# Performance work log

Measured on AMD Instinct MI355X. Metric: run time of the kernel, lower is better.

## Reference

```python
import jax, jax.numpy as jnp
import numpy as np

WS = 7           # window size
N = WS * WS      # tokens per window = 49
C = 128          # embed dim
H = 4            # heads
HD = C // H      # head dim = 32
NW = 64          # num windows (mask leading dim)
B = 4096         # total windows = outer_batch * NW


def _relative_indexes():
    ch = np.arange(WS)
    cw = np.arange(WS)
    coords = np.stack(np.meshgrid(ch, cw, indexing='ij')).reshape(2, -1)  # [2, N]
    rel = coords[:, :, None] - coords[:, None, :]                          # [2, N, N]
    rel = rel.transpose(1, 2, 0)
    rel[:, :, 0] += WS - 1
    rel[:, :, 1] += WS - 1
    rel[:, :, 0] *= 2 * WS - 1
    return jnp.asarray(rel.sum(-1), dtype=jnp.int32)                       # [N, N]


def setup_inputs() -> dict:
    key = jax.random.key(0)
    ks = jax.random.split(key, 10)
    s = 0.02
    return {
        'query': jax.random.normal(ks[0], (B, N, C), jnp.float32),
        'source': jax.random.normal(ks[1], (B, N, C), jnp.float32),
        'mask': jnp.zeros((NW, N, N), jnp.float32),
        'q_w': jax.random.normal(ks[2], (C, C), jnp.float32) * s,
        'q_b': jnp.zeros((C,), jnp.float32),
        'kv_w': jax.random.normal(ks[3], (C, 2 * C), jnp.float32) * s,
        'kv_b': jnp.zeros((2 * C,), jnp.float32),
        'proj_w': jax.random.normal(ks[4], (C, C), jnp.float32) * s,
        'proj_b': jnp.zeros((C,), jnp.float32),
        'bias_table': jax.random.normal(ks[5], ((2 * WS - 1) ** 2, H), jnp.float32) * s,
        'rel_idx': _relative_indexes(),
    }


def reference(query, source, mask, q_w, q_b, kv_w, kv_b, proj_w, proj_b, bias_table, rel_idx):
    scale = HD ** -0.5
    q = query @ q_w + q_b                       # [B, N, C]
    kv = source @ kv_w + kv_b                   # [B, N, 2C]
    k, v = kv[..., :C], kv[..., C:]
    # [B, N, H, HD] -> [B, H, N, HD]
    q = q.reshape(B, N, H, HD).transpose(0, 2, 1, 3) * scale
    k = k.reshape(B, N, H, HD).transpose(0, 2, 1, 3)
    v = v.reshape(B, N, H, HD).transpose(0, 2, 1, 3)
    attn = jnp.einsum('bhnd,bhmd->bhnm', q, k)  # [B, H, N, N]
    # gathered relative positional bias: [1, H, N, N]
    bias = bias_table[rel_idx.reshape(-1)].reshape(N, N, H).transpose(2, 0, 1)[None]
    attn = attn + bias
    # mask: [NW, N, N] broadcast over outer batch and heads
    attn = attn.reshape(-1, NW, H, N, N) + mask[None, :, None]
    attn = attn.reshape(B, H, N, N)
    attn = jax.nn.softmax(attn, axis=-1)
    x = jnp.einsum('bhnm,bhmd->bnhd', attn, v).reshape(B, N, C)
    return x @ proj_w + proj_b
```

## Files before the change

### kernel.cpp

```cpp
#include <hip/hip_runtime.h>
#include <hip/hip_bf16.h>

#define NN 49
#define CC 128
#define HH 4
#define NWIN 64
#define BB 4096
#define QSCALE 0.17677669529663687f

typedef __attribute__((ext_vector_type(8))) short bf16x8;
typedef __attribute__((ext_vector_type(4))) float f32x4;
typedef unsigned short u16;
typedef unsigned int u32;

union U8 { u32 u[4]; bf16x8 v; };

__device__ __forceinline__ u16 f2b(float f) {
    __hip_bfloat16 h = __float2bfloat16(f);
    return __builtin_bit_cast(u16, h);
}
__device__ __forceinline__ float b2f(u16 u) { return __uint_as_float(((u32)u) << 16); }
__device__ __forceinline__ u32 cvtpk(float lo, float hi) {
    u32 r;
    asm("v_cvt_pk_bf16_f32 %0, %1, %2" : "=v"(r) : "v"(lo), "v"(hi));
    return r;
}
__device__ __forceinline__ uint2 pack4(float a, float b, float c, float d) {
    uint2 r;
    r.x = cvtpk(a, b);
    r.y = cvtpk(c, d);
    return r;
}
__device__ __forceinline__ f32x4 mfma16(bf16x8 a, bf16x8 b, f32x4 c) {
    return __builtin_amdgcn_mfma_f32_16x16x32_bf16(a, b, c, 0, 0, 0);
}
__device__ __forceinline__ char* adr256(u16* base, int row, int byte) {
    return (char*)base + row * 256 + (byte ^ ((row & 7) << 4));
}
__device__ __forceinline__ char* adr128(u16* base, int row, int byte) {
    return (char*)base + row * 128 + (byte ^ ((row & 7) << 4));
}

__global__ void prep_cbt(const float* __restrict__ bias_table, const int* __restrict__ rel_idx,
                         const float* __restrict__ mask, u16* __restrict__ cbt) {
    int idx = blockIdx.x * blockDim.x + threadIdx.x;
    int m = idx & 63, i = (idx >> 6) & 63, h = (idx >> 12) & 3, wv = idx >> 14;
    if (wv >= NWIN) return;
    float v = -1e9f;
    if (m < NN && i < NN)
        v = bias_table[rel_idx[i * NN + m] * HH + h] + mask[(wv * NN + i) * NN + m];
    cbt[idx] = f2b(v);
}

__global__ void prep_w(const float* __restrict__ qw, const float* __restrict__ qb,
                       const float* __restrict__ kvw, const float* __restrict__ pjw,
                       u16* __restrict__ qwp, u16* __restrict__ kvwp,
                       u16* __restrict__ pjwp, float* __restrict__ qbs) {
    int idx = blockIdx.x * blockDim.x + threadIdx.x;
    if (idx < 16384) {
        int i = idx & 7, lane = (idx >> 3) & 63, kt = (idx >> 9) & 3, nt = idx >> 11;
        int k = 32 * kt + 8 * (lane >> 4) + i, n = 16 * nt + (lane & 15);
        qwp[idx] = f2b(qw[k * CC + n] * QSCALE);
    } else if (idx < 49152) {
        int j = idx - 16384;
        int i = j & 7, lane = (j >> 3) & 63, kt = (j >> 9) & 3, nt = j >> 11;
        int k = 32 * kt + 8 * (lane >> 4) + i, n = 16 * nt + (lane & 15);
        kvwp[j] = f2b(kvw[k * 2 * CC + n]);
    } else if (idx < 65536) {
        int j = idx - 49152;
        int i = j & 7, lane = (j >> 3) & 63, kt = (j >> 9) & 3, nt = j >> 11;
        int k = 32 * kt + 8 * (lane >> 4) + i, n = 16 * nt + (lane & 15);
        pjwp[j] = f2b(pjw[k * CC + n]);
    } else if (idx < 65664) {
        int j = idx - 65536;
        qbs[j] = qb[j] * QSCALE;
    }
}

__global__ __launch_bounds__(512, 2)
void wmha_main(const float* __restrict__ query, const float* __restrict__ source,
               const u16* __restrict__ qwp, const u16* __restrict__ kvwp,
               const u16* __restrict__ pjwp, const float* __restrict__ qbs,
               const float* __restrict__ kv_b, const float* __restrict__ proj_b,
               const u16* __restrict__ cbt, float* __restrict__ out) {
    __shared__ u16 lds[40960];
    u16* SQ = lds;
    u16* SS = lds + 8192;
    u16* Qb = lds + 16384;
    u16* Kb = lds + 24576;
    u16* VT = lds + 32768;
    const int t = threadIdx.x;
    const int b = blockIdx.x;
    const int w = t >> 6, lane = t & 63;
    const int lq = lane & 15, qd = lane >> 4;
    const int mw = w >> 2;
    const int nw = w & 3;
    const int h = w >> 1;
    const int half = w & 1;

    {
        const int row = t >> 3, qu = t & 7;
        const size_t gbase = (size_t)b * NN * CC + row * CC + qu * 8;
        #pragma unroll
        for (int j = 0; j < 2; ++j) {
            U8 vq, vs;
            if (row < NN) {
                const float4* q4 = (const float4*)(query + gbase) + 16 * j;
                const float4* s4 = (const float4*)(source + gbase) + 16 * j;
                float4 a0 = q4[0], a1 = q4[1], c0 = s4[0], c1 = s4[1];
                vq.u[0] = cvtpk(a0.x, a0.y); vq.u[1] = cvtpk(a0.z, a0.w);
                vq.u[2] = cvtpk(a1.x, a1.y); vq.u[3] = cvtpk(a1.z, a1.w);
                vs.u[0] = cvtpk(c0.x, c0.y); vs.u[1] = cvtpk(c0.z, c0.w);
                vs.u[2] = cvtpk(c1.x, c1.y); vs.u[3] = cvtpk(c1.z, c1.w);
            } else {
                vq.u[0] = vq.u[1] = vq.u[2] = vq.u[3] = 0;
                vs.u[0] = vs.u[1] = vs.u[2] = vs.u[3] = 0;
            }
            *(bf16x8*)adr256(SQ, row, qu * 16 + 128 * j) = vq.v;
            *(bf16x8*)adr256(SS, row, qu * 16 + 128 * j) = vs.v;
        }
    }
    bf16x8 bwq[2][4];
    #pragma unroll
    for (int n2 = 0; n2 < 2; ++n2)
        #pragma unroll
        for (int kt = 0; kt < 4; ++kt)
            bwq[n2][kt] = *(const bf16x8*)(qwp + (((nw + 4 * n2) * 4 + kt) * 64 + lane) * 8);
    __syncthreads();

    {
        f32x4 acc[2][2] = {};
        #pragma unroll
        for (int m2 = 0; m2 < 2; ++m2) {
            bf16x8 a[4];
            #pragma unroll
            for (int kt = 0; kt < 4; ++kt)
                a[kt] = *(const bf16x8*)adr256(SQ, (2 * mw + m2) * 16 + lq, kt * 64 + qd * 16);
            __builtin_amdgcn_s_setprio(1);
            #pragma unroll
            for (int n2 = 0; n2 < 2; ++n2)
                #pragma unroll
                for (int kt = 0; kt < 4; ++kt)
                    acc[m2][n2] = mfma16(bwq[n2][kt], a[kt], acc[m2][n2]);
            __builtin_amdgcn_s_setprio(0);
        }
        #pragma unroll
        for (int n2 = 0; n2 < 2; ++n2) {
            const int cb0 = 16 * (nw + 4 * n2) + 4 * qd;
            const float4 bia = *(const float4*)(qbs + cb0);
            #pragma unroll
            for (int m2 = 0; m2 < 2; ++m2) {
                const int tok = (2 * mw + m2) * 16 + lq;
                uint2 pk = pack4(acc[m2][n2][0] + bia.x, acc[m2][n2][1] + bia.y,
                                 acc[m2][n2][2] + bia.z, acc[m2][n2][3] + bia.w);
                *(uint2*)adr256(Qb, tok, 2 * cb0) = pk;
            }
        }
    }
    {
        bf16x8 as[2][4];
        #pragma unroll
        for (int m2 = 0; m2 < 2; ++m2)
            #pragma unroll
            for (int kt = 0; kt < 4; ++kt)
                as[m2][kt] = *(const bf16x8*)adr256(SS, (2 * mw + m2) * 16 + lq, kt * 64 + qd * 16);
        {
            bf16x8 bwk[2][4];
            #pragma unroll
            for (int n2 = 0; n2 < 2; ++n2)
                #pragma unroll
                for (int kt = 0; kt < 4; ++kt)
                    bwk[n2][kt] = *(const bf16x8*)(kvwp + (((nw + 4 * n2) * 4 + kt) * 64 + lane) * 8);
            f32x4 acc[2][2] = {};
            __builtin_amdgcn_s_setprio(1);
            #pragma unroll
            for (int m2 = 0; m2 < 2; ++m2)
                #pragma unroll
                for (int n2 = 0; n2 < 2; ++n2)
                    #pragma unroll
                    for (int kt = 0; kt < 4; ++kt)
                        acc[m2][n2] = mfma16(bwk[n2][kt], as[m2][kt], acc[m2][n2]);
            __builtin_amdgcn_s_setprio(0);
            #pragma unroll
            for (int n2 = 0; n2 < 2; ++n2) {
                const int cb0 = 16 * (nw + 4 * n2) + 4 * qd;
                const float4 bia = *(const float4*)(kv_b + cb0);
                #pragma unroll
                for (int m2 = 0; m2 < 2; ++m2) {
                    const int tok = (2 * mw + m2) * 16 + lq;
                    uint2 pk = pack4(acc[m2][n2][0] + bia.x, acc[m2][n2][1] + bia.y,
                                     acc[m2][n2][2] + bia.z, acc[m2][n2][3] + bia.w);
                    *(uint2*)adr256(Kb, tok, 2 * cb0) = pk;
                }
            }
        }
        {
            bf16x8 bwv[2][4];
            #pragma unroll
            for (int n2 = 0; n2 < 2; ++n2)
                #pragma unroll
                for (int kt = 0; kt < 4; ++kt)
                    bwv[n2][kt] = *(const bf16x8*)(kvwp + (((8 + nw + 4 * n2) * 4 + kt) * 64 + lane) * 8);
            f32x4 acc[2][2] = {};
            __builtin_amdgcn_s_setprio(1);
            #pragma unroll
            for (int m2 = 0; m2 < 2; ++m2)
                #pragma unroll
                for (int n2 = 0; n2 < 2; ++n2)
                    #pragma unroll
                    for (int kt = 0; kt < 4; ++kt)
                        acc[m2][n2] = mfma16(as[m2][kt], bwv[n2][kt], acc[m2][n2]);
            __builtin_amdgcn_s_setprio(0);
            #pragma unroll
            for (int n2 = 0; n2 < 2; ++n2) {
                const int dim = 16 * (nw + 4 * n2) + lq;
                const float bias = kv_b[CC + dim];
                #pragma unroll
                for (int m2 = 0; m2 < 2; ++m2) {
                    uint2 pk = pack4(acc[m2][n2][0] + bias, acc[m2][n2][1] + bias,
                                     acc[m2][n2][2] + bias, acc[m2][n2][3] + bias);
                    *(uint2*)adr128(VT, dim, 2 * ((2 * mw + m2) * 16 + qd * 4)) = pk;
                }
            }
        }
    }
    __syncthreads();

    f32x4 s[2][4];
    bf16x8 vf[2][2];
    {
        bf16x8 kf[4], qf[2];
        #pragma unroll
        for (int a = 0; a < 4; ++a)
            kf[a] = *(const bf16x8*)adr256(Kb, a * 16 + lq, h * 64 + qd * 16);
        #pragma unroll
        for (int i = 0; i < 2; ++i)
            qf[i] = *(const bf16x8*)adr256(Qb, (2 * half + i) * 16 + lq, h * 64 + qd * 16);
        __builtin_amdgcn_s_setprio(1);
        #pragma unroll
        for (int i = 0; i < 2; ++i) {
            f32x4 z = {0.f, 0.f, 0.f, 0.f};
            #pragma unroll
            for (int a = 0; a < 4; ++a)
                s[i][a] = mfma16(kf[a], qf[i], z);
        }
        __builtin_amdgcn_s_setprio(0);
        #pragma unroll
        for (int dt = 0; dt < 2; ++dt)
            #pragma unroll
            for (int kt = 0; kt < 2; ++kt)
                vf[dt][kt] = *(const bf16x8*)adr128(VT, h * 32 + dt * 16 + lq, kt * 64 + qd * 16);
    }
    uint2 cbr[2][4];
    {
        const u16* cbb = cbt + ((size_t)((b & (NWIN - 1)) * HH + h) << 12);
        #pragma unroll
        for (int i = 0; i < 2; ++i)
            #pragma unroll
            for (int a = 0; a < 4; ++a)
                cbr[i][a] = *(const uint2*)(cbb + ((2 * half + i) * 16 + lq) * 64 + a * 16 + qd * 4);
    }
    __syncthreads();

    {
        u16* pb0 = Qb + w * 1024;
        u16* pb1 = Kb + w * 1024;
        float smv[2];
        #pragma unroll
        for (int i = 0; i < 2; ++i) {
            #pragma unroll
            for (int a = 0; a < 3; ++a) {
                s[i][a][0] += b2f((u16)(cbr[i][a].x & 0xffffu));
                s[i][a][1] += b2f((u16)(cbr[i][a].x >> 16));
                s[i][a][2] += b2f((u16)(cbr[i][a].y & 0xffffu));
                s[i][a][3] += b2f((u16)(cbr[i][a].y >> 16));
            }
            s[i][3][0] += b2f((u16)(cbr[i][3].x & 0xffffu));
            uint2 pk[4];
            float sm = 0.f;
            #pragma unroll
            for (int a = 0; a < 3; ++a) {
                float p0 = __expf(s[i][a][0]), p1 = __expf(s[i][a][1]);
                float p2 = __expf(s[i][a][2]), p3 = __expf(s[i][a][3]);
                pk[a].x = cvtpk(p0, p1);
                pk[a].y = cvtpk(p2, p3);
                sm += (p0 + p1) + (p2 + p3);
            }
            float p30 = __expf(s[i][3][0]);
            pk[3].x = cvtpk(p30, 0.f);
            pk[3].y = 0u;
            sm += p30;
            smv[i] = sm;
            u16* pb = i ? pb1 : pb0;
            #pragma unroll
            for (int a = 0; a < 4; ++a)
                *(uint2*)adr128(pb, lq, 32 * a + 8 * qd) = pk[a];
        }
        asm volatile("s_waitcnt lgkmcnt(0)" ::: "memory");
        __builtin_amdgcn_sched_barrier(0);
        float t0 = smv[0] + __shfl_xor(smv[0], 16);
        float t1 = smv[1] + __shfl_xor(smv[1], 16);
        float inv[2];
        inv[0] = 1.f / (t0 + __shfl_xor(t0, 32));
        inv[1] = 1.f / (t1 + __shfl_xor(t1, 32));
        f32x4 o[2][2] = {};
        __builtin_amdgcn_s_setprio(1);
        #pragma unroll
        for (int kt = 0; kt < 2; ++kt) {
            bf16x8 pf0 = *(const bf16x8*)adr128(pb0, lq, 64 * kt + 16 * qd);
            bf16x8 pf1 = *(const bf16x8*)adr128(pb1, lq, 64 * kt + 16 * qd);
            #pragma unroll
            for (int dt = 0; dt < 2; ++dt) {
                o[0][dt] = mfma16(vf[dt][kt], pf0, o[0][dt]);
                o[1][dt] = mfma16(vf[dt][kt], pf1, o[1][dt]);
            }
        }
        __builtin_amdgcn_s_setprio(0);
        #pragma unroll
        for (int i = 0; i < 2; ++i)
            #pragma unroll
            for (int dt = 0; dt < 2; ++dt) {
                uint2 px = pack4(o[i][dt][0] * inv[i], o[i][dt][1] * inv[i],
                                 o[i][dt][2] * inv[i], o[i][dt][3] * inv[i]);
                *(uint2*)adr256(SQ, (2 * half + i) * 16 + lq, 64 * h + 32 * dt + 8 * qd) = px;
            }
    }

    {
        bf16x8 bw[2][4];
        #pragma unroll
        for (int n2 = 0; n2 < 2; ++n2)
            #pragma unroll
            for (int kt = 0; kt < 4; ++kt)
                bw[n2][kt] = *(const bf16x8*)(pjwp + (((nw + 4 * n2) * 4 + kt) * 64 + lane) * 8);
        __syncthreads();
        f32x4 acc[2][2] = {};
        #pragma unroll
        for (int m2 = 0; m2 < 2; ++m2) {
            bf16x8 a[4];
            #pragma unroll
            for (int kt = 0; kt < 4; ++kt)
                a[kt] = *(const bf16x8*)adr256(SQ, (2 * mw + m2) * 16 + lq, kt * 64 + qd * 16);
            __builtin_amdgcn_s_setprio(1);
            #pragma unroll
            for (int n2 = 0; n2 < 2; ++n2)
                #pragma unroll
                for (int kt = 0; kt < 4; ++kt)
                    acc[m2][n2] = mfma16(bw[n2][kt], a[kt], acc[m2][n2]);
            __builtin_amdgcn_s_setprio(0);
        }
        float* outb = out + (size_t)b * NN * CC;
        #pragma unroll
        for (int n2 = 0; n2 < 2; ++n2) {
            const int cb0 = 16 * (nw + 4 * n2) + 4 * qd;
            const float4 bia = *(const float4*)(proj_b + cb0);
            #pragma unroll
            for (int m2 = 0; m2 < 2; ++m2) {
                const int tok = (2 * mw + m2) * 16 + lq;
                if (tok < NN) {
                    float4 vst;
                    vst.x = acc[m2][n2][0] + bia.x;
                    vst.y = acc[m2][n2][1] + bia.y;
                    vst.z = acc[m2][n2][2] + bia.z;
                    vst.w = acc[m2][n2][3] + bia.w;
                    *(float4*)(outb + tok * CC + cb0) = vst;
                }
            }
        }
    }
}

extern "C" void kernel_launch(void* const* d_in, const int* in_sizes, int n_in,
                              void* d_out, int out_size, void* d_ws, size_t ws_size,
                              hipStream_t stream) {
    const float* query      = (const float*)d_in[0];
    const float* source     = (const float*)d_in[1];
    const float* mask       = (const float*)d_in[2];
    const float* q_w        = (const float*)d_in[3];
    const float* q_b        = (const float*)d_in[4];
    const float* kv_w       = (const float*)d_in[5];
    const float* kv_b       = (const float*)d_in[6];
    const float* proj_w     = (const float*)d_in[7];
    const float* proj_b     = (const float*)d_in[8];
    const float* bias_table = (const float*)d_in[9];
    const int*   rel_idx    = (const int*)d_in[10];
    float* out = (float*)d_out;

    u16* cbt   = (u16*)d_ws;
    u16* qwp   = cbt + 1048576;
    u16* kvwp  = qwp + 16384;
    u16* pjwp  = kvwp + 32768;
    float* qbs = (float*)(pjwp + 16384);

    prep_cbt<<<4096, 256, 0, stream>>>(bias_table, rel_idx, mask, cbt);
    prep_w<<<257, 256, 0, stream>>>(q_w, q_b, kv_w, proj_w, qwp, kvwp, pjwp, qbs);
    wmha_main<<<BB, 512, 0, stream>>>(query, source, qwp, kvwp, pjwp, qbs,
                                      kv_b, proj_b, cbt, out);
}
```

Before: 122.3 us.

## Make blocks persistent over 8 windows with register prefetch of next window

Each block now loops over 8 windows instead of one, and the grid shrinks to 512 blocks. During each window, the next window's query and source rows are loaded into registers so the global load latency overlaps with the softmax and PV stage. The attention output is now staged in VT so SQ/SS can be refilled early. This adds register pressure from the prefetch buffers and extra syncs. With only 512 blocks, the machine may be underfilled and load per CU may be uneven.

```diff
diff --git a/kernel.cpp b/kernel.cpp
--- a/kernel.cpp
+++ b/kernel.cpp
@@ -6,6 +6,7 @@
 #define HH 4
 #define NWIN 64
 #define BB 4096
+#define WPB 8
 #define QSCALE 0.17677669529663687f
 
 typedef __attribute__((ext_vector_type(8))) short bf16x8;
@@ -90,21 +91,21 @@
     u16* Kb = lds + 24576;
     u16* VT = lds + 32768;
     const int t = threadIdx.x;
-    const int b = blockIdx.x;
     const int w = t >> 6, lane = t & 63;
     const int lq = lane & 15, qd = lane >> 4;
     const int mw = w >> 2;
     const int nw = w & 3;
     const int h = w >> 1;
     const int half = w & 1;
+    const int srow = t >> 3, qu = t & 7;
+    const int b0 = blockIdx.x * WPB;
 
     {
-        const int row = t >> 3, qu = t & 7;
-        const size_t gbase = (size_t)b * NN * CC + row * CC + qu * 8;
+        const size_t gbase = (size_t)b0 * NN * CC + srow * CC + qu * 8;
         #pragma unroll
         for (int j = 0; j < 2; ++j) {
             U8 vq, vs;
-            if (row < NN) {
+            if (srow < NN) {
                 const float4* q4 = (const float4*)(query + gbase) + 16 * j;
                 const float4* s4 = (const float4*)(source + gbase) + 16 * j;
                 float4 a0 = q4[0], a1 = q4[1], c0 = s4[0], c1 = s4[1];
@@ -116,257 +117,292 @@
                 vq.u[0] = vq.u[1] = vq.u[2] = vq.u[3] = 0;
                 vs.u[0] = vs.u[1] = vs.u[2] = vs.u[3] = 0;
             }
-            *(bf16x8*)adr256(SQ, row, qu * 16 + 128 * j) = vq.v;
-            *(bf16x8*)adr256(SS, row, qu * 16 + 128 * j) = vs.v;
+            *(bf16x8*)adr256(SQ, srow, qu * 16 + 128 * j) = vq.v;
+            *(bf16x8*)adr256(SS, srow, qu * 16 + 128 * j) = vs.v;
         }
     }
-    bf16x8 bwq[2][4];
-    #pragma unroll
-    for (int n2 = 0; n2 < 2; ++n2)
-        #pragma unroll
-        for (int kt = 0; kt < 4; ++kt)
-            bwq[n2][kt] = *(const bf16x8*)(qwp + (((nw + 4 * n2) * 4 + kt) * 64 + lane) * 8);
     __syncthreads();
 
-    {
-        f32x4 acc[2][2] = {};
-        #pragma unroll
-        for (int m2 = 0; m2 < 2; ++m2) {
-            bf16x8 a[4];
-            #pragma unroll
-            for (int kt = 0; kt < 4; ++kt)
-                a[kt] = *(const bf16x8*)adr256(SQ, (2 * mw + m2) * 16 + lq, kt * 64 + qd * 16);
-            __builtin_amdgcn_s_setprio(1);
+    for (int it = 0; it < WPB; ++it) {
+        const int b = b0 + it;
+        const bool pf = (it + 1 < WPB);
+
+        {
+            bf16x8 bwq[2][4];
             #pragma unroll
             for (int n2 = 0; n2 < 2; ++n2)
                 #pragma unroll
                 for (int kt = 0; kt < 4; ++kt)
-                    acc[m2][n2] = mfma16(bwq[n2][kt], a[kt], acc[m2][n2]);
-            __builtin_amdgcn_s_setprio(0);
-        }
-        #pragma unroll
-        for (int n2 = 0; n2 < 2; ++n2) {
-            const int cb0 = 16 * (nw + 4 * n2) + 4 * qd;
-            const float4 bia = *(const float4*)(qbs + cb0);
+                    bwq[n2][kt] = *(const bf16x8*)(qwp + (((nw + 4 * n2) * 4 + kt) * 64 + lane) * 8);
+            f32x4 acc[2][2] = {};
             #pragma unroll
             for (int m2 = 0; m2 < 2; ++m2) {
-                const int tok = (2 * mw + m2) * 16 + lq;
-                uint2 pk = pack4(acc[m2][n2][0] + bia.x, acc[m2][n2][1] + bia.y,
-                                 acc[m2][n2][2] + bia.z, acc[m2][n2][3] + bia.w);
-                *(uint2*)adr256(Qb, tok, 2 * cb0) = pk;
-            }
-        }
-    }
-    {
-        bf16x8 as[2][4];
-        #pragma unroll
-        for (int m2 = 0; m2 < 2; ++m2)
-            #pragma unroll
-            for (int kt = 0; kt < 4; ++kt)
-                as[m2][kt] = *(const bf16x8*)adr256(SS, (2 * mw + m2) * 16 + lq, kt * 64 + qd * 16);
-        {
-            bf16x8 bwk[2][4];
-            #pragma unroll
-            for (int n2 = 0; n2 < 2; ++n2)
+                bf16x8 a[4];
                 #pragma unroll
                 for (int kt = 0; kt < 4; ++kt)
-                    bwk[n2][kt] = *(const bf16x8*)(kvwp + (((nw + 4 * n2) * 4 + kt) * 64 + lane) * 8);
-            f32x4 acc[2][2] = {};
-            __builtin_amdgcn_s_setprio(1);
-            #pragma unroll
-            for (int m2 = 0; m2 < 2; ++m2)
+                    a[kt] = *(const bf16x8*)adr256(SQ, (2 * mw + m2) * 16 + lq, kt * 64 + qd * 16);
+                __builtin_amdgcn_s_setprio(1);
                 #pragma unroll
                 for (int n2 = 0; n2 < 2; ++n2)
                     #pragma unroll
                     for (int kt = 0; kt < 4; ++kt)
-                        acc[m2][n2] = mfma16(bwk[n2][kt], as[m2][kt], acc[m2][n2]);
-            __builtin_amdgcn_s_setprio(0);
+                        acc[m2][n2] = mfma16(bwq[n2][kt], a[kt], acc[m2][n2]);
+                __builtin_amdgcn_s_setprio(0);
+            }
             #pragma unroll
             for (int n2 = 0; n2 < 2; ++n2) {
                 const int cb0 = 16 * (nw + 4 * n2) + 4 * qd;
-                const float4 bia = *(const float4*)(kv_b + cb0);
+                const float4 bia = *(const float4*)(qbs + cb0);
                 #pragma unroll
                 for (int m2 = 0; m2 < 2; ++m2) {
                     const int tok = (2 * mw + m2) * 16 + lq;
                     uint2 pk = pack4(acc[m2][n2][0] + bia.x, acc[m2][n2][1] + bia.y,
                                      acc[m2][n2][2] + bia.z, acc[m2][n2][3] + bia.w);
-                    *(uint2*)adr256(Kb, tok, 2 * cb0) = pk;
-                }
-            }
-        }
-        {
-            bf16x8 bwv[2][4];
+                    *(uint2*)adr256(Qb, tok, 2 * cb0) = pk;
+                }
+            }
+        }
+        {
+            bf16x8 as[2][4];
+            #pragma unroll
+            for (int m2 = 0; m2 < 2; ++m2)
+                #pragma unroll
+                for (int kt = 0; kt < 4; ++kt)
+                    as[m2][kt] = *(const bf16x8*)adr256(SS, (2 * mw + m2) * 16 + lq, kt * 64 + qd * 16);
+            {
+                bf16x8 bwk[2][4];
+                #pragma unroll
+                for (int n2 = 0; n2 < 2; ++n2)
+                    #pragma unroll
+                    for (int kt = 0; kt < 4; ++kt)
+                        bwk[n2][kt] = *(const bf16x8*)(kvwp + (((nw + 4 * n2) * 4 + kt) * 64 + lane) * 8);
+                f32x4 acc[2][2] = {};
+                __builtin_amdgcn_s_setprio(1);
+                #pragma unroll
+                for (int m2 = 0; m2 < 2; ++m2)
+                    #pragma unroll
+                    for (int n2 = 0; n2 < 2; ++n2)
+                        #pragma unroll
+                        for (int kt = 0; kt < 4; ++kt)
+                            acc[m2][n2] = mfma16(bwk[n2][kt], as[m2][kt], acc[m2][n2]);
+                __builtin_amdgcn_s_setprio(0);
+                #pragma unroll
+                for (int n2 = 0; n2 < 2; ++n2) {
+                    const int cb0 = 16 * (nw + 4 * n2) + 4 * qd;
+                    const float4 bia = *(const float4*)(kv_b + cb0);
+                    #pragma unroll
+                    for (int m2 = 0; m2 < 2; ++m2) {
+                        const int tok = (2 * mw + m2) * 16 + lq;
+                        uint2 pk = pack4(acc[m2][n2][0] + bia.x, acc[m2][n2][1] + bia.y,
+                                         acc[m2][n2][2] + bia.z, acc[m2][n2][3] + bia.w);
+                        *(uint2*)adr256(Kb, tok, 2 * cb0) = pk;
+                    }
+                }
+            }
+            {
+                bf16x8 bwv[2][4];
+                #pragma unroll
+                for (int n2 = 0; n2 < 2; ++n2)
+                    #pragma unroll
+                    for (int kt = 0; kt < 4; ++kt)
+                        bwv[n2][kt] = *(const bf16x8*)(kvwp + (((8 + nw + 4 * n2) * 4 + kt) * 64 + lane) * 8);
+                f32x4 acc[2][2] = {};
+                __builtin_amdgcn_s_setprio(1);
+                #pragma unroll
+                for (int m2 = 0; m2 < 2; ++m2)
+                    #pragma unroll
+                    for (int n2 = 0; n2 < 2; ++n2)
+                        #pragma unroll
+                        for (int kt = 0; kt < 4; ++kt)
+                            acc[m2][n2] = mfma16(as[m2][kt], bwv[n2][kt], acc[m2][n2]);
+                __builtin_amdgcn_s_setprio(0);
+                #pragma unroll
+                for (int n2 = 0; n2 < 2; ++n2) {
+                    const int dim = 16 * (nw + 4 * n2) + lq;
+                    const float bias = kv_b[CC + dim];
+                    #pragma unroll
+                    for (int m2 = 0; m2 < 2; ++m2) {
+                        uint2 pk = pack4(acc[m2][n2][0] + bias, acc[m2][n2][1] + bias,
+                                         acc[m2][n2][2] + bias, acc[m2][n2][3] + bias);
+                        *(uint2*)adr128(VT, dim, 2 * ((2 * mw + m2) * 16 + qd * 4)) = pk;
+                    }
+                }
+            }
+        }
+        __syncthreads();
+
+        f32x4 s[2][4];
+        bf16x8 vf[2][2];
+        {
+            bf16x8 kf[4], qf[2];
+            #pragma unroll
+            for (int a = 0; a < 4; ++a)
+                kf[a] = *(const bf16x8*)adr256(Kb, a * 16 + lq, h * 64 + qd * 16);
+            #pragma unroll
+            for (int i = 0; i < 2; ++i)
+                qf[i] = *(const bf16x8*)adr256(Qb, (2 * half + i) * 16 + lq, h * 64 + qd * 16);
+            __builtin_amdgcn_s_setprio(1);
+            #pragma unroll
+            for (int i = 0; i < 2; ++i) {
+                f32x4 z = {0.f, 0.f, 0.f, 0.f};
+                #pragma unroll
+                for (int a = 0; a < 4; ++a)
+                    s[i][a] = mfma16(kf[a], qf[i], z);
+            }
+            __builtin_amdgcn_s_setprio(0);
+            #pragma unroll
+            for (int dt = 0; dt < 2; ++dt)
+                #pragma unroll
+                for (int kt = 0; kt < 2; ++kt)
+                    vf[dt][kt] = *(const bf16x8*)adr128(VT, h * 32 + dt * 16 + lq, kt * 64 + qd * 16);
+        }
+        uint2 cbr[2][4];
+        {
+            const u16* cbb = cbt + ((size_t)((b & (NWIN - 1)) * HH + h) << 12);
+            #pragma unroll
+            for (int i = 0; i < 2; ++i)
+                #pragma unroll
+                for (int a = 0; a < 4; ++a)
+                    cbr[i][a] = *(const uint2*)(cbb + ((2 * half + i) * 16 + lq) * 64 + a * 16 + qd * 4);
+        }
+        float4 nq0, nq1, nq2, nq3, ns0, ns1, ns2, ns3;
+        if (pf && srow < NN) {
+            const float4* qn = (const float4*)(query + (size_t)(b + 1) * NN * CC + srow * CC + qu * 8);
+            const float4* sn = (const float4*)(source + (size_t)(b + 1) * NN * CC + srow * CC + qu * 8);
+            nq0 = qn[0]; nq1 = qn[1]; nq2 = qn[16]; nq3 = qn[17];
+            ns0 = sn[0]; ns1 = sn[1]; ns2 = sn[16]; ns3 = sn[17];
+        }
+        __syncthreads();
+
+        {
+            u16* pb0 = Qb + w * 1024;
+            u16* pb1 = Kb + w * 1024;
+            float smv[2];
+            #pragma unroll
+            for (int i = 0; i < 2; ++i) {
+                #pragma unroll
+                for (int a = 0; a < 3; ++a) {
+                    s[i][a][0] += b2f((u16)(cbr[i][a].x & 0xffffu));
+                    s[i][a][1] += b2f((u16)(cbr[i][a].x >> 16));
+                    s[i][a][2] += b2f((u16)(cbr[i][a].y & 0xffffu));
+                    s[i][a][3] += b2f((u16)(cbr[i][a].y >> 16));
+                }
+                s[i][3][0] += b2f((u16)(cbr[i][3].x & 0xffffu));
+                uint2 pk[4];
+                float sm = 0.f;
+                #pragma unroll
+                for (int a = 0; a < 3; ++a) {
+                    float p0 = __expf(s[i][a][0]), p1 = __expf(s[i][a][1]);
+                    float p2 = __expf(s[i][a][2]), p3 = __expf(s[i][a][3]);
+                    pk[a].x = cvtpk(p0, p1);
+                    pk[a].y = cvtpk(p2, p3);
+                    sm += (p0 + p1) + (p2 + p3);
+                }
+                float p30 = __expf(s[i][3][0]);
+                pk[3].x = cvtpk(p30, 0.f);
+                pk[3].y = 0u;
+                sm += p30;
+                smv[i] = sm;
+                u16* pb = i ? pb1 : pb0;
+                #pragma unroll
+                for (int a = 0; a < 4; ++a)
+                    *(uint2*)adr128(pb, lq, 32 * a + 8 * qd) = pk[a];
+            }
+            asm volatile("s_waitcnt lgkmcnt(0)" ::: "memory");
+            __builtin_amdgcn_sched_barrier(0);
+            float t0 = smv[0] + __shfl_xor(smv[0], 16);
+            float t1 = smv[1] + __shfl_xor(smv[1], 16);
+            float inv[2];
+            inv[0] = 1.f / (t0 + __shfl_xor(t0, 32));
+            inv[1] = 1.f / (t1 + __shfl_xor(t1, 32));
+            f32x4 o[2][2] = {};
+            __builtin_amdgcn_s_setprio(1);
+            #pragma unroll
+            for (int kt = 0; kt < 2; ++kt) {
+                bf16x8 pf0 = *(const bf16x8*)adr128(pb0, lq, 64 * kt + 16 * qd);
+                bf16x8 pf1 = *(const bf16x8*)adr128(pb1, lq, 64 * kt + 16 * qd);
+                #pragma unroll
+                for (int dt = 0; dt < 2; ++dt) {
+                    o[0][dt] = mfma16(vf[dt][kt], pf0, o[0][dt]);
+                    o[1][dt] = mfma16(vf[dt][kt], pf1, o[1][dt]);
+                }
+            }
+            __builtin_amdgcn_s_setprio(0);
+            #pragma unroll
+            for (int i = 0; i < 2; ++i)
+                #pragma unroll
+                for (int dt = 0; dt < 2; ++dt) {
+                    uint2 px = pack4(o[i][dt][0] * inv[i], o[i][dt][1] * inv[i],
+                                     o[i][dt][2] * inv[i], o[i][dt][3] * inv[i]);
+                    *(uint2*)adr256(VT, (2 * half + i) * 16 + lq, 64 * h + 32 * dt + 8 * qd) = px;
+                }
+        }
+        if (pf) {
+            U8 vq, vs;
+            if (srow < NN) {
+                vq.u[0] = cvtpk(nq0.x, nq0.y); vq.u[1] = cvtpk(nq0.z, nq0.w);
+                vq.u[2] = cvtpk(nq1.x, nq1.y); vq.u[3] = cvtpk(nq1.z, nq1.w);
+                vs.u[0] = cvtpk(ns0.x, ns0.y); vs.u[1] = cvtpk(ns0.z, ns0.w);
+                vs.u[2] = cvtpk(ns1.x, ns1.y); vs.u[3] = cvtpk(ns1.z, ns1.w);
+            } else {
+                vq.u[0] = vq.u[1] = vq.u[2] = vq.u[3] = 0;
+                vs.u[0] = vs.u[1] = vs.u[2] = vs.u[3] = 0;
+            }
+            *(bf16x8*)adr256(SQ, srow, qu * 16) = vq.v;
+            *(bf16x8*)adr256(SS, srow, qu * 16) = vs.v;
+            if (srow < NN) {
+                vq.u[0] = cvtpk(nq2.x, nq2.y); vq.u[1] = cvtpk(nq2.z, nq2.w);
+                vq.u[2] = cvtpk(nq3.x, nq3.y); vq.u[3] = cvtpk(nq3.z, nq3.w);
+                vs.u[0] = cvtpk(ns2.x, ns2.y); vs.u[1] = cvtpk(ns2.z, ns2.w);
+                vs.u[2] = cvtpk(ns3.x, ns3.y); vs.u[3] = cvtpk(ns3.z, ns3.w);
+            }
+            *(bf16x8*)adr256(SQ, srow, qu * 16 + 128) = vq.v;
+            *(bf16x8*)adr256(SS, srow, qu * 16 + 128) = vs.v;
+        }
+
+        {
+            bf16x8 bw[2][4];
             #pragma unroll
             for (int n2 = 0; n2 < 2; ++n2)
                 #pragma unroll
                 for (int kt = 0; kt < 4; ++kt)
-                    bwv[n2][kt] = *(const bf16x8*)(kvwp + (((8 + nw + 4 * n2) * 4 + kt) * 64 + lane) * 8);
+                    bw[n2][kt] = *(const bf16x8*)(pjwp + (((nw + 4 * n2) * 4 + kt) * 64 + lane) * 8);
+            __syncthreads();
             f32x4 acc[2][2] = {};
-            __builtin_amdgcn_s_setprio(1);
-            #pragma unroll
-            for (int m2 = 0; m2 < 2; ++m2)
+            #pragma unroll
+            for (int m2 = 0; m2 < 2; ++m2) {
+                bf16x8 a[4];
+                #pragma unroll
+                for (int kt = 0; kt < 4; ++kt)
+                    a[kt] = *(const bf16x8*)adr256(VT, (2 * mw + m2) * 16 + lq, kt * 64 + qd * 16);
+                __builtin_amdgcn_s_setprio(1);
                 #pragma unroll
                 for (int n2 = 0; n2 < 2; ++n2)
                     #pragma unroll
                     for (int kt = 0; kt < 4; ++kt)
-                        acc[m2][n2] = mfma16(as[m2][kt], bwv[n2][kt], acc[m2][n2]);
-            __builtin_amdgcn_s_setprio(0);
+                        acc[m2][n2] = mfma16(bw[n2][kt], a[kt], acc[m2][n2]);
+                __builtin_amdgcn_s_setprio(0);
+            }
+            float* outb = out + (size_t)b * NN * CC;
             #pragma unroll
             for (int n2 = 0; n2 < 2; ++n2) {
-                const int dim = 16 * (nw + 4 * n2) + lq;
-                const float bias = kv_b[CC + dim];
+                const int cb0 = 16 * (nw + 4 * n2) + 4 * qd;
+                const float4 bia = *(const float4*)(proj_b + cb0);
                 #pragma unroll
                 for (int m2 = 0; m2 < 2; ++m2) {
-                    uint2 pk = pack4(acc[m2][n2][0] + bias, acc[m2][n2][1] + bias,
-                                     acc[m2][n2][2] + bias, acc[m2][n2][3] + bias);
-                    *(uint2*)adr128(VT, dim, 2 * ((2 * mw + m2) * 16 + qd * 4)) = pk;
-                }
-            }
-        }
-    }
-    __syncthreads();
-
-    f32x4 s[2][4];
-    bf16x8 vf[2][2];
-    {
-        bf16x8 kf[4], qf[2];
-        #pragma unroll
-        for (int a = 0; a < 4; ++a)
-            kf[a] = *(const bf16x8*)adr256(Kb, a * 16 + lq, h * 64 + qd * 16);
-        #pragma unroll
-        for (int i = 0; i < 2; ++i)
-            qf[i] = *(const bf16x8*)adr256(Qb, (2 * half + i) * 16 + lq, h * 64 + qd * 16);
-        __builtin_amdgcn_s_setprio(1);
-        #pragma unroll
-        for (int i = 0; i < 2; ++i) {
-            f32x4 z = {0.f, 0.f, 0.f, 0.f};
-            #pragma unroll
-            for (int a = 0; a < 4; ++a)
-                s[i][a] = mfma16(kf[a], qf[i], z);
-        }
-        __builtin_amdgcn_s_setprio(0);
-        #pragma unroll
-        for (int dt = 0; dt < 2; ++dt)
-            #pragma unroll
-            for (int kt = 0; kt < 2; ++kt)
-                vf[dt][kt] = *(const bf16x8*)adr128(VT, h * 32 + dt * 16 + lq, kt * 64 + qd * 16);
-    }
-    uint2 cbr[2][4];
-    {
-        const u16* cbb = cbt + ((size_t)((b & (NWIN - 1)) * HH + h) << 12);
-        #pragma unroll
-        for (int i = 0; i < 2; ++i)
-            #pragma unroll
-            for (int a = 0; a < 4; ++a)
-                cbr[i][a] = *(const uint2*)(cbb + ((2 * half + i) * 16 + lq) * 64 + a * 16 + qd * 4);
-    }
-    __syncthreads();
-
-    {
-        u16* pb0 = Qb + w * 1024;
-        u16* pb1 = Kb + w * 1024;
-        float smv[2];
-        #pragma unroll
-        for (int i = 0; i < 2; ++i) {
-            #pragma unroll
-            for (int a = 0; a < 3; ++a) {
-                s[i][a][0] += b2f((u16)(cbr[i][a].x & 0xffffu));
-                s[i][a][1] += b2f((u16)(cbr[i][a].x >> 16));
-                s[i][a][2] += b2f((u16)(cbr[i][a].y & 0xffffu));
-                s[i][a][3] += b2f((u16)(cbr[i][a].y >> 16));
-            }
-            s[i][3][0] += b2f((u16)(cbr[i][3].x & 0xffffu));
-            uint2 pk[4];
-            float sm = 0.f;
-            #pragma unroll
-            for (int a = 0; a < 3; ++a) {
-                float p0 = __expf(s[i][a][0]), p1 = __expf(s[i][a][1]);
-                float p2 = __expf(s[i][a][2]), p3 = __expf(s[i][a][3]);
-                pk[a].x = cvtpk(p0, p1);
-                pk[a].y = cvtpk(p2, p3);
-                sm += (p0 + p1) + (p2 + p3);
-            }
-            float p30 = __expf(s[i][3][0]);
-            pk[3].x = cvtpk(p30, 0.f);
-            pk[3].y = 0u;
-            sm += p30;
-            smv[i] = sm;
-            u16* pb = i ? pb1 : pb0;
-            #pragma unroll
-            for (int a = 0; a < 4; ++a)
-                *(uint2*)adr128(pb, lq, 32 * a + 8 * qd) = pk[a];
-        }
-        asm volatile("s_waitcnt lgkmcnt(0)" ::: "memory");
-        __builtin_amdgcn_sched_barrier(0);
-        float t0 = smv[0] + __shfl_xor(smv[0], 16);
-        float t1 = smv[1] + __shfl_xor(smv[1], 16);
-        float inv[2];
-        inv[0] = 1.f / (t0 + __shfl_xor(t0, 32));
-        inv[1] = 1.f / (t1 + __shfl_xor(t1, 32));
-        f32x4 o[2][2] = {};
-        __builtin_amdgcn_s_setprio(1);
-        #pragma unroll
-        for (int kt = 0; kt < 2; ++kt) {
-            bf16x8 pf0 = *(const bf16x8*)adr128(pb0, lq, 64 * kt + 16 * qd);
-            bf16x8 pf1 = *(const bf16x8*)adr128(pb1, lq, 64 * kt + 16 * qd);
-            #pragma unroll
-            for (int dt = 0; dt < 2; ++dt) {
-                o[0][dt] = mfma16(vf[dt][kt], pf0, o[0][dt]);
-                o[1][dt] = mfma16(vf[dt][kt], pf1, o[1][dt]);
-            }
-        }
-        __builtin_amdgcn_s_setprio(0);
-        #pragma unroll
-        for (int i = 0; i < 2; ++i)
-            #pragma unroll
-            for (int dt = 0; dt < 2; ++dt) {
-                uint2 px = pack4(o[i][dt][0] * inv[i], o[i][dt][1] * inv[i],
-                                 o[i][dt][2] * inv[i], o[i][dt][3] * inv[i]);
-                *(uint2*)adr256(SQ, (2 * half + i) * 16 + lq, 64 * h + 32 * dt + 8 * qd) = px;
-            }
-    }
-
-    {
-        bf16x8 bw[2][4];
-        #pragma unroll
-        for (int n2 = 0; n2 < 2; ++n2)
-            #pragma unroll
-            for (int kt = 0; kt < 4; ++kt)
-                bw[n2][kt] = *(const bf16x8*)(pjwp + (((nw + 4 * n2) * 4 + kt) * 64 + lane) * 8);
-        __syncthreads();
-        f32x4 acc[2][2] = {};
-        #pragma unroll
-        for (int m2 = 0; m2 < 2; ++m2) {
-            bf16x8 a[4];
-            #pragma unroll
-            for (int kt = 0; kt < 4; ++kt)
-                a[kt] = *(const bf16x8*)adr256(SQ, (2 * mw + m2) * 16 + lq, kt * 64 + qd * 16);
-            __builtin_amdgcn_s_setprio(1);
-            #pragma unroll
-            for (int n2 = 0; n2 < 2; ++n2)
-                #pragma unroll
-                for (int kt = 0; kt < 4; ++kt)
-                    acc[m2][n2] = mfma16(bw[n2][kt], a[kt], acc[m2][n2]);
-            __builtin_amdgcn_s_setprio(0);
-        }
-        float* outb = out + (size_t)b * NN * CC;
-        #pragma unroll
-        for (int n2 = 0; n2 < 2; ++n2) {
-            const int cb0 = 16 * (nw + 4 * n2) + 4 * qd;
-            const float4 bia = *(const float4*)(proj_b + cb0);
-            #pragma unroll
-            for (int m2 = 0; m2 < 2; ++m2) {
-                const int tok = (2 * mw + m2) * 16 + lq;
-                if (tok < NN) {
-                    float4 vst;
-                    vst.x = acc[m2][n2][0] + bia.x;
-                    vst.y = acc[m2][n2][1] + bia.y;
-                    vst.z = acc[m2][n2][2] + bia.z;
-                    vst.w = acc[m2][n2][3] + bia.w;
-                    *(float4*)(outb + tok * CC + cb0) = vst;
-                }
-            }
-        }
+                    const int tok = (2 * mw + m2) * 16 + lq;
+                    if (tok < NN) {
+                        float4 vst;
+                        vst.x = acc[m2][n2][0] + bia.x;
+                        vst.y = acc[m2][n2][1] + bia.y;
+                        vst.z = acc[m2][n2][2] + bia.z;
+                        vst.w = acc[m2][n2][3] + bia.w;
+                        *(float4*)(outb + tok * CC + cb0) = vst;
+                    }
+                }
+            }
+        }
+        if (pf) __syncthreads();
     }
 }
 
@@ -394,6 +430,6 @@
 
     prep_cbt<<<4096, 256, 0, stream>>>(bias_table, rel_idx, mask, cbt);
     prep_w<<<257, 256, 0, stream>>>(q_w, q_b, kv_w, proj_w, qwp, kvwp, pjwp, qbs);
-    wmha_main<<<BB, 512, 0, stream>>>(query, source, qwp, kvwp, pjwp, qbs,
-                                      kv_b, proj_b, cbt, out);
-}
+    wmha_main<<<BB / WPB, 512, 0, stream>>>(query, source, qwp, kvwp, pjwp, qbs,
+                                            kv_b, proj_b, cbt, out);
+}
```

New measurement: 134.2 us. +9.8%, slower.
